# Kernel optimization log

Measured on AMD Instinct MI355X. Metric: run time of the kernel, lower is better.

## Reference

```python
import jax, jax.numpy as jnp
import numpy as np
from jax import lax

H = 128
N = 4096


def gru_cell(x, h, Wih, Whh, bih, bhh):
    # PyTorch GRU gate order: r, z, n
    gi = x @ Wih + bih
    gh = h @ Whh + bhh
    ir, iz, inn = jnp.split(gi, 3, axis=-1)
    hr, hz, hn = jnp.split(gh, 3, axis=-1)
    r = jax.nn.sigmoid(ir + hr)
    z = jax.nn.sigmoid(iz + hz)
    n = jnp.tanh(inn + r * hn)
    return (1.0 - z) * n + z * h


def setup_inputs() -> dict:
    key = jax.random.key(0)
    ks = jax.random.split(key, 32)
    s = 0.02
    rn = lambda k, shp, sc=s: (jax.random.normal(k, shp, jnp.float32) * sc)
    inp = {
        'boxes_feature': jax.random.normal(ks[0], (1, N, 1024), jnp.float32),
        'boxes_box_score': jax.random.normal(ks[1], (1, N, 2560), jnp.float32),
        'boxes_box': jax.random.normal(ks[2], (1, N, 320), jnp.float32),
        'boxes_label': jax.random.uniform(ks[3], (1, N), jnp.float32),
        'boxes_weight': jax.random.uniform(ks[4], (1, N), jnp.float32),
        'boxes_num': N,
        'W_appear': rn(ks[5], (1024, H)), 'b_appear': jnp.zeros((H,), jnp.float32),
        'W_s1': rn(ks[6], (2560, 512)), 'b_s1': jnp.zeros((512,), jnp.float32),
        'W_s2': rn(ks[7], (512, H)), 'b_s2': jnp.zeros((H,), jnp.float32),
        'W_box': rn(ks[8], (320, H)), 'b_box': jnp.zeros((H,), jnp.float32),
        'W_all': rn(ks[9], (3 * H, H)), 'b_all': jnp.zeros((H,), jnp.float32),
        'enc_Wih': rn(ks[10], (H, 3 * H)), 'enc_Whh': rn(ks[11], (H, 3 * H)),
        'enc_bih': jnp.zeros((3 * H,), jnp.float32), 'enc_bhh': jnp.zeros((3 * H,), jnp.float32),
        'dec_Wih': rn(ks[12], (H, 3 * H)), 'dec_Whh': rn(ks[13], (H, 3 * H)),
        'dec_bih': jnp.zeros((3 * H,), jnp.float32), 'dec_bhh': jnp.zeros((3 * H,), jnp.float32),
        'W_attn': rn(ks[14], (2 * H, 1)), 'b_attn': jnp.zeros((1,), jnp.float32),
        'W_comb': rn(ks[15], (2 * H, H)), 'b_comb': jnp.zeros((H,), jnp.float32),
        'W_out': rn(ks[16], (H, 1)), 'b_out': jnp.zeros((1,), jnp.float32),
    }
    return inp


def reference(boxes_feature, boxes_box_score, boxes_box, boxes_label, boxes_weight, boxes_num,
              W_appear, b_appear, W_s1, b_s1, W_s2, b_s2, W_box, b_box, W_all, b_all,
              enc_Wih, enc_Whh, enc_bih, enc_bhh, dec_Wih, dec_Whh, dec_bih, dec_bhh,
              W_attn, b_attn, W_comb, b_comb, W_out, b_out):
    n = boxes_num
    h = W_appear.shape[1]
    # per-proposal feature fusion
    ef = jax.nn.relu(boxes_feature[0, :n] @ W_appear + b_appear)            # [N, h]
    es = jax.nn.relu((boxes_box_score[0, :n] @ W_s1 + b_s1) @ W_s2 + b_s2)  # [N, h]
    eb = jax.nn.relu(boxes_box[0, :n] @ W_box + b_box)                       # [N, h]
    X = jax.nn.relu(jnp.concatenate([ef, es, eb], axis=1) @ W_all + b_all)   # [N, h]

    # encoder GRU over proposals (batch=1)
    def enc_step(hc, x):
        hn = gru_cell(x, hc, enc_Wih, enc_Whh, enc_bih, enc_bhh)
        return hn, hn
    h0 = jnp.zeros((h,), X.dtype)
    h_enc, E = lax.scan(enc_step, h0, X)  # E: [N, h]

    # Bahdanau-style attention; NOTE: original softmaxes each [1,1] score over
    # dim=1, so every weight is exactly 1.0. We keep softmax for faithful grads.
    Xw = X @ W_attn[h:]  # [N, 1], constant part of the attn score

    def dec_step(hc, x):
        scores = hc @ W_attn[:h] + b_attn + Xw          # [N, 1]
        w = jax.nn.softmax(scores, axis=1)              # [N, 1] == all ones
        applied = w[:, 0] @ E                           # [h]
        din = jax.nn.relu(jnp.concatenate([x, applied]) @ W_comb + b_comb)
        hn = gru_cell(din, hc, dec_Wih, dec_Whh, dec_bih, dec_bhh)
        return hn, hn

    _, D = lax.scan(dec_step, h_enc, X)  # D: [N, h]
    output = jax.nn.sigmoid(D @ W_out + b_out)  # [N, 1]
    return output, boxes_label[0, :n], boxes_weight[0, :n]
```

## Files before the change

### kernel.cpp

```cpp
#include <hip/hip_runtime.h>
#include <hip/hip_bf16.h>
#include <math.h>

#define NBOX 4096
#define HDIM 128
#define G3   384
#define PF   8

typedef _Float16 half2v __attribute__((ext_vector_type(2)));
typedef short bf16x8 __attribute__((ext_vector_type(8)));
typedef float f32x4 __attribute__((ext_vector_type(4)));
#define LDK 40

__device__ __forceinline__ float sigm(float x) { return 1.f / (1.f + expf(-x)); }
__device__ __forceinline__ float sigm_fast(float x) {
    return __builtin_amdgcn_rcpf(1.f + __expf(-x));
}
__device__ __forceinline__ float tanh_fast(float x) {
    x = fminf(15.f, fmaxf(-15.f, x));
    const float e2 = __expf(2.f * x);
    return (e2 - 1.f) * __builtin_amdgcn_rcpf(e2 + 1.f);
}
__device__ __forceinline__ float bcast_q1(float x) {
    return __int_as_float(__builtin_amdgcn_mov_dpp(__float_as_int(x), 0x55, 0xF, 0xF, false));
}
__device__ __forceinline__ float bcast_q3(float x) {
    return __int_as_float(__builtin_amdgcn_mov_dpp(__float_as_int(x), 0xFF, 0xF, 0xF, false));
}
__device__ __forceinline__ float qsum(float v) {
    v += __int_as_float(__builtin_amdgcn_mov_dpp(__float_as_int(v), 0xB1, 0xF, 0xF, false));
    v += __int_as_float(__builtin_amdgcn_mov_dpp(__float_as_int(v), 0x4E, 0xF, 0xF, false));
    return v;
}
__device__ __forceinline__ float fdot2(unsigned int h2, unsigned int w2, float acc) {
    return __builtin_amdgcn_fdot2(__builtin_bit_cast(half2v, h2),
                                  __builtin_bit_cast(half2v, w2), acc, false);
}
__device__ __forceinline__ void bar_lds() {
    asm volatile("s_waitcnt lgkmcnt(0)\n\ts_barrier" ::: "memory");
}
__device__ __forceinline__ unsigned short f2bf(float x) {
    return __builtin_bit_cast(unsigned short, __float2bfloat16(x));
}

__global__ __launch_bounds__(256) void gemm_f32(
    const float* __restrict__ A, const float* __restrict__ B,
    const float* __restrict__ bias, float* __restrict__ C,
    int M, int N, int K, int ldc, int act)
{
    __shared__ float As[16][132];
    __shared__ float Bs[16][68];
    const int tid = threadIdx.x;
    const int m0 = blockIdx.y * 128;
    const int n0 = blockIdx.x * 64;
    const int ak = tid & 15, am = tid >> 4;
    const int bn = tid & 63, bk = tid >> 6;
    const int tx = tid & 15, ty = tid >> 4;
    float acc[8][4] = {};
    for (int k0 = 0; k0 < K; k0 += 16) {
#pragma unroll
        for (int r = 0; r < 8; ++r)
            As[ak][am + 16 * r] = A[(size_t)(m0 + am + 16 * r) * K + k0 + ak];
#pragma unroll
        for (int r = 0; r < 4; ++r)
            Bs[bk + 4 * r][bn] = B[(size_t)(k0 + bk + 4 * r) * N + n0 + bn];
        __syncthreads();
#pragma unroll
        for (int k = 0; k < 16; ++k) {
            float4 a0 = *(const float4*)&As[k][ty * 8];
            float4 a1 = *(const float4*)&As[k][ty * 8 + 4];
            float4 b0 = *(const float4*)&Bs[k][tx * 4];
            float a[8] = {a0.x, a0.y, a0.z, a0.w, a1.x, a1.y, a1.z, a1.w};
            float b[4] = {b0.x, b0.y, b0.z, b0.w};
#pragma unroll
            for (int i = 0; i < 8; ++i)
#pragma unroll
                for (int j = 0; j < 4; ++j)
                    acc[i][j] = fmaf(a[i], b[j], acc[i][j]);
        }
        __syncthreads();
    }
#pragma unroll
    for (int i = 0; i < 8; ++i) {
        const int m = m0 + ty * 8 + i;
#pragma unroll
        for (int j = 0; j < 4; ++j) {
            const int n = n0 + tx * 4 + j;
            float v = acc[i][j] + bias[n];
            if (act) v = fmaxf(v, 0.f);
            C[(size_t)m * ldc + n] = v;
        }
    }
}

__global__ __launch_bounds__(256) void conv_bt(
    const float* __restrict__ B, unsigned short* __restrict__ Bt, int K, int N)
{
    const int id = blockIdx.x * 256 + threadIdx.x;
    if (id < K * N) {
        const int n = id / K, k = id % K;
        Bt[(size_t)n * K + k] = f2bf(B[(size_t)k * N + n]);
    }
}

__global__ __launch_bounds__(256) void gemm_bf16t(
    const float* __restrict__ A, const unsigned short* __restrict__ Bt,
    const float* __restrict__ bias, float* __restrict__ C,
    int M, int N, int K, int ldc, int act)
{
    __shared__ unsigned short As[128][LDK];
    __shared__ unsigned short Bs[128][LDK];
    const int tid = threadIdx.x;
    const int m0 = blockIdx.y * 128, n0 = blockIdx.x * 128;
    const int wv = tid >> 6, lane = tid & 63;
    const int wr = (wv >> 1) * 64, wc = (wv & 1) * 64;
    const int lr = lane & 15, lk = lane >> 4;
    const int sm = tid >> 1, skh = (tid & 1) * 16;
    f32x4 acc[4][4] = {};
    for (int k0 = 0; k0 < K; k0 += 32) {
        const float* ga = &A[(size_t)(m0 + sm) * K + k0 + skh];
        float4 f0 = *(const float4*)(ga + 0);
        float4 f1 = *(const float4*)(ga + 4);
        float4 f2 = *(const float4*)(ga + 8);
        float4 f3 = *(const float4*)(ga + 12);
        const float fa[16] = {f0.x,f0.y,f0.z,f0.w, f1.x,f1.y,f1.z,f1.w,
                              f2.x,f2.y,f2.z,f2.w, f3.x,f3.y,f3.z,f3.w};
        unsigned int pk[8];
#pragma unroll
        for (int e = 0; e < 8; ++e)
            pk[e] = (unsigned int)f2bf(fa[2*e]) | ((unsigned int)f2bf(fa[2*e+1]) << 16);
        *(uint4*)&As[sm][skh]     = make_uint4(pk[0], pk[1], pk[2], pk[3]);
        *(uint4*)&As[sm][skh + 8] = make_uint4(pk[4], pk[5], pk[6], pk[7]);
        const uint4* gb = (const uint4*)&Bt[(size_t)(n0 + sm) * K + k0 + skh];
        *(uint4*)&Bs[sm][skh]     = gb[0];
        *(uint4*)&Bs[sm][skh + 8] = gb[1];
        __syncthreads();
        bf16x8 af[4], bfr[4];
#pragma unroll
        for (int f = 0; f < 4; ++f) {
            af[f]  = *(const bf16x8*)&As[wr + f * 16 + lr][lk * 8];
            bfr[f] = *(const bf16x8*)&Bs[wc + f * 16 + lr][lk * 8];
        }
#pragma unroll
        for (int i = 0; i < 4; ++i)
#pragma unroll
            for (int j = 0; j < 4; ++j)
                acc[i][j] = __builtin_amdgcn_mfma_f32_16x16x32_bf16(
                    af[i], bfr[j], acc[i][j], 0, 0, 0);
        __syncthreads();
    }
#pragma unroll
    for (int i = 0; i < 4; ++i)
#pragma unroll
        for (int j = 0; j < 4; ++j)
#pragma unroll
            for (int r = 0; r < 4; ++r) {
                const int row = m0 + wr + i * 16 + lk * 4 + r;
                const int col = n0 + wc + j * 16 + lr;
                float v = acc[i][j][r] + bias[col];
                if (act) v = fmaxf(v, 0.f);
                C[(size_t)row * ldc + col] = v;
            }
}

__global__ __launch_bounds__(256)
__attribute__((amdgpu_waves_per_eu(1, 1)))
void gru_scan(
    const float* __restrict__ GI, const float* __restrict__ Whh,
    const float* __restrict__ bhh, const float* __restrict__ h0,
    double* __restrict__ esum_out, float* __restrict__ hfinal_out,
    float* __restrict__ D_out, int T)
{
    __shared__ unsigned short h16[2][HDIM];
    const int tid = threadIdx.x;
    const int j = tid >> 2;
    const int g = tid & 3;
    const int qa = 2 * j, qb = 2 * j + 1;
    const int myq = (g & 2) ? qb : qa;
    const int colS = ((g & 1) ? HDIM : 0) + myq;
    const int colT = 2 * HDIM + myq;
    unsigned int w[96];
#pragma unroll
    for (int c6 = 0; c6 < 6; ++c6) {
        const int cc = (c6 % 3) * HDIM + ((c6 < 3) ? qa : qb);
#pragma unroll
        for (int p2 = 0; p2 < 16; ++p2) {
            const int k = 32 * g + 2 * p2;
            const _Float16 lo = (_Float16)Whh[(size_t)k * G3 + cc];
            const _Float16 hi = (_Float16)Whh[(size_t)(k + 1) * G3 + cc];
            w[c6 * 16 + p2] = (unsigned int)__builtin_bit_cast(unsigned short, lo)
                            | ((unsigned int)__builtin_bit_cast(unsigned short, hi) << 16);
        }
    }
#pragma unroll
    for (int p = 0; p < 96; ++p) asm volatile("" : "+v"(w[p]));
    const float bS = bhh[colS];
    const float bT = bhh[colT];
    if (tid < HDIM)
        h16[0][tid] = __builtin_bit_cast(unsigned short,
                                         (_Float16)(h0 ? h0[tid] : 0.f));
    float hp = (float)(_Float16)(h0 ? h0[myq] : 0.f);
    double esum = 0.0;
    float gS[PF], gT[PF], gSn[PF], gTn[PF];
#pragma unroll
    for (int p = 0; p < PF; ++p) {
        gS[p] = GI[(size_t)p * G3 + colS];
        gT[p] = GI[(size_t)p * G3 + colT];
    }
    __syncthreads();
    for (int t0 = 0; t0 < T; t0 += PF) {
#pragma unroll
        for (int p = 0; p < PF; ++p) {
            gSn[p] = GI[(size_t)(t0 + PF + p) * G3 + colS];
            gTn[p] = GI[(size_t)(t0 + PF + p) * G3 + colT];
        }
#pragma unroll
        for (int p = 0; p < PF; ++p) {
            const int t = t0 + p;
            const uint4* hb = (const uint4*)h16[t & 1];
            uint4 uu[4];
#pragma unroll
            for (int pp = 0; pp < 4; ++pp) uu[pp] = hb[4 * g + pp];
            float s0 = 0.f, s1 = 0.f, s2 = 0.f, s3 = 0.f, s4 = 0.f, s5 = 0.f;
#pragma unroll
            for (int pp = 0; pp < 4; ++pp) {
                const unsigned int x[4] = {uu[pp].x, uu[pp].y, uu[pp].z, uu[pp].w};
#pragma unroll
                for (int i2 = 0; i2 < 4; ++i2) {
                    const int pi = 4 * pp + i2;
                    s0 = fdot2(x[i2], w[pi], s0);
                    s1 = fdot2(x[i2], w[16 + pi], s1);
                    s2 = fdot2(x[i2], w[32 + pi], s2);
                    s3 = fdot2(x[i2], w[48 + pi], s3);
                    s4 = fdot2(x[i2], w[64 + pi], s4);
                    s5 = fdot2(x[i2], w[80 + pi], s5);
                }
            }
            s0 = qsum(s0); s1 = qsum(s1); s2 = qsum(s2);
            s3 = qsum(s3); s4 = qsum(s4); s5 = qsum(s5);
            const float ghS = ((g & 2) ? ((g & 1) ? s4 : s3)
                                       : ((g & 1) ? s1 : s0)) + bS;
            const float ghT = ((g & 2) ? s5 : s2) + bT;
            const float s = sigm_fast(gS[p] + ghS);
            const float n = tanh_fast(gT[p] + s * ghT);
            const float z1 = bcast_q1(s);
            const float z3 = bcast_q3(s);
            const float z = (g & 2) ? z3 : z1;
            const float hn = z * (hp - n) + n;
            if (!(g & 1)) {
                h16[(t + 1) & 1][myq] =
                    __builtin_bit_cast(unsigned short, (_Float16)hn);
                esum += (double)hn;
                if (D_out) D_out[(size_t)t * HDIM + myq] = hn;
            }
            hp = (float)(_Float16)hn;
            bar_lds();
        }
#pragma unroll
        for (int p = 0; p < PF; ++p) { gS[p] = gSn[p]; gT[p] = gTn[p]; }
    }
    if (!(g & 1)) {
        if (esum_out) esum_out[myq] = esum;
        if (hfinal_out) hfinal_out[myq] = hp;
    }
}

__global__ void prep_dec(const double* __restrict__ esum, const float* __restrict__ W_comb,
                         const float* __restrict__ b_comb, float* __restrict__ c2)
{
    __shared__ double es[HDIM];
    const int j = threadIdx.x;
    es[j] = esum[j];
    __syncthreads();
    double acc = (double)b_comb[j];
    for (int k = 0; k < HDIM; ++k)
        acc += es[k] * (double)W_comb[(HDIM + k) * HDIM + j];
    c2[j] = (float)acc;
}

__global__ __launch_bounds__(256) void out_row(
    const float* __restrict__ D, const float* __restrict__ Wout,
    const float* __restrict__ b_out, float* __restrict__ out)
{
    const int row = (blockIdx.x * 256 + threadIdx.x) >> 6;
    const int lane = threadIdx.x & 63;
    float v = D[(size_t)row * HDIM + lane] * Wout[lane]
            + D[(size_t)row * HDIM + 64 + lane] * Wout[64 + lane];
#pragma unroll
    for (int s = 32; s > 0; s >>= 1) v += __shfl_down(v, s);
    if (lane == 0) out[row] = sigm(v + b_out[0]);
}

__global__ void copy_lw(const float* __restrict__ lab, const float* __restrict__ wt,
                        float* __restrict__ out)
{
    const int i = blockIdx.x * 256 + threadIdx.x;
    if (i < NBOX) { out[NBOX + i] = lab[i]; out[2 * NBOX + i] = wt[i]; }
}

extern "C" void kernel_launch(void* const* d_in, const int* in_sizes, int n_in,
                              void* d_out, int out_size, void* d_ws, size_t ws_size,
                              hipStream_t stream)
{
    const float* boxes_feature = (const float*)d_in[0];
    const float* boxes_score   = (const float*)d_in[1];
    const float* boxes_box     = (const float*)d_in[2];
    const float* boxes_label   = (const float*)d_in[3];
    const float* boxes_weight  = (const float*)d_in[4];
    const float* W_appear = (const float*)d_in[6];
    const float* b_appear = (const float*)d_in[7];
    const float* W_s1     = (const float*)d_in[8];
    const float* b_s1     = (const float*)d_in[9];
    const float* W_s2     = (const float*)d_in[10];
    const float* b_s2     = (const float*)d_in[11];
    const float* W_box    = (const float*)d_in[12];
    const float* b_box    = (const float*)d_in[13];
    const float* W_all    = (const float*)d_in[14];
    const float* b_all    = (const float*)d_in[15];
    const float* enc_Wih  = (const float*)d_in[16];
    const float* enc_Whh  = (const float*)d_in[17];
    const float* enc_bih  = (const float*)d_in[18];
    const float* enc_bhh  = (const float*)d_in[19];
    const float* dec_Wih  = (const float*)d_in[20];
    const float* dec_Whh  = (const float*)d_in[21];
    const float* dec_bih  = (const float*)d_in[22];
    const float* dec_bhh  = (const float*)d_in[23];
    const float* W_comb   = (const float*)d_in[26];
    const float* b_comb   = (const float*)d_in[27];
    const float* W_out    = (const float*)d_in[28];
    const float* b_out    = (const float*)d_in[29];

    float* out = (float*)d_out;
    float* ws = (float*)d_ws;
    size_t o = 0;
    float* T1   = ws + o; o += (size_t)NBOX * 512;
    float* XCAT = ws + o; o += (size_t)NBOX * G3;
    float* X    = ws + o; o += (size_t)NBOX * HDIM;
    float* GIE  = ws + o; o += (size_t)(NBOX + PF) * G3;
    float* GID  = ws + o; o += (size_t)(NBOX + PF) * G3;
    float* DIN  = ws + o; o += (size_t)NBOX * HDIM;
    float* D    = ws + o; o += (size_t)NBOX * HDIM;
    o = (o + 1) & ~(size_t)1;
    double* esum = (double*)(ws + o); o += 256;
    float* henc = ws + o; o += 128;
    float* c2   = ws + o; o += 128;
    unsigned short* Wt_bf = (unsigned short*)GIE;

    conv_bt<<<(2560 * 512 + 255) / 256, 256, 0, stream>>>(W_s1, Wt_bf, 2560, 512);
    gemm_bf16t<<<dim3(512 / 128, NBOX / 128), 256, 0, stream>>>(
        boxes_score, Wt_bf, b_s1, T1, NBOX, 512, 2560, 512, 0);
    gemm_f32<<<dim3(HDIM / 64, NBOX / 128), 256, 0, stream>>>(
        boxes_feature, W_appear, b_appear, XCAT + 0, NBOX, HDIM, 1024, G3, 1);
    gemm_f32<<<dim3(HDIM / 64, NBOX / 128), 256, 0, stream>>>(
        T1, W_s2, b_s2, XCAT + HDIM, NBOX, HDIM, 512, G3, 1);
    gemm_f32<<<dim3(HDIM / 64, NBOX / 128), 256, 0, stream>>>(
        boxes_box, W_box, b_box, XCAT + 2 * HDIM, NBOX, HDIM, 320, G3, 1);
    gemm_f32<<<dim3(HDIM / 64, NBOX / 128), 256, 0, stream>>>(
        XCAT, W_all, b_all, X, NBOX, HDIM, G3, HDIM, 1);

    gemm_f32<<<dim3(G3 / 64, NBOX / 128), 256, 0, stream>>>(
        X, enc_Wih, enc_bih, GIE, NBOX, G3, HDIM, G3, 0);
    gru_scan<<<1, 256, 0, stream>>>(GIE, enc_Whh, enc_bhh, nullptr,
                                    esum, henc, nullptr, NBOX);

    prep_dec<<<1, 128, 0, stream>>>(esum, W_comb, b_comb, c2);
    gemm_f32<<<dim3(HDIM / 64, NBOX / 128), 256, 0, stream>>>(
        X, W_comb, c2, DIN, NBOX, HDIM, HDIM, HDIM, 1);
    gemm_f32<<<dim3(G3 / 64, NBOX / 128), 256, 0, stream>>>(
        DIN, dec_Wih, dec_bih, GID, NBOX, G3, HDIM, G3, 0);

    gru_scan<<<1, 256, 0, stream>>>(GID, dec_Whh, dec_bhh, henc,
                                    nullptr, nullptr, D, NBOX);

    out_row<<<NBOX / 4, 256, 0, stream>>>(D, W_out, b_out, out);
    copy_lw<<<NBOX / 256, 256, 0, stream>>>(boxes_label, boxes_weight, out);
}
```

Measured before the change: 3.851 ms.

## Move all projection GEMMs to bf16 MFMA path and fuse epilogue kernels

Replaces every fp32 SIMT GEMM (appearance, score, box, combine, input-gate projections) with the existing bf16 transposed-weight MFMA GEMM, adding transposition/conversion launches for each weight into reused workspace buffers. It also merges the output-row and label/weight copy kernels into one launch. This targets the feed-forward GEMM time and launch overhead, at the cost of bf16 precision in the projections and extra conversion launches; the sequential GRU scans are unchanged.

```diff
diff --git a/kernel.cpp b/kernel.cpp
--- a/kernel.cpp
+++ b/kernel.cpp
@@ -41,56 +41,6 @@
 }
 __device__ __forceinline__ unsigned short f2bf(float x) {
     return __builtin_bit_cast(unsigned short, __float2bfloat16(x));
-}
-
-__global__ __launch_bounds__(256) void gemm_f32(
-    const float* __restrict__ A, const float* __restrict__ B,
-    const float* __restrict__ bias, float* __restrict__ C,
-    int M, int N, int K, int ldc, int act)
-{
-    __shared__ float As[16][132];
-    __shared__ float Bs[16][68];
-    const int tid = threadIdx.x;
-    const int m0 = blockIdx.y * 128;
-    const int n0 = blockIdx.x * 64;
-    const int ak = tid & 15, am = tid >> 4;
-    const int bn = tid & 63, bk = tid >> 6;
-    const int tx = tid & 15, ty = tid >> 4;
-    float acc[8][4] = {};
-    for (int k0 = 0; k0 < K; k0 += 16) {
-#pragma unroll
-        for (int r = 0; r < 8; ++r)
-            As[ak][am + 16 * r] = A[(size_t)(m0 + am + 16 * r) * K + k0 + ak];
-#pragma unroll
-        for (int r = 0; r < 4; ++r)
-            Bs[bk + 4 * r][bn] = B[(size_t)(k0 + bk + 4 * r) * N + n0 + bn];
-        __syncthreads();
-#pragma unroll
-        for (int k = 0; k < 16; ++k) {
-            float4 a0 = *(const float4*)&As[k][ty * 8];
-            float4 a1 = *(const float4*)&As[k][ty * 8 + 4];
-            float4 b0 = *(const float4*)&Bs[k][tx * 4];
-            float a[8] = {a0.x, a0.y, a0.z, a0.w, a1.x, a1.y, a1.z, a1.w};
-            float b[4] = {b0.x, b0.y, b0.z, b0.w};
-#pragma unroll
-            for (int i = 0; i < 8; ++i)
-#pragma unroll
-                for (int j = 0; j < 4; ++j)
-                    acc[i][j] = fmaf(a[i], b[j], acc[i][j]);
-        }
-        __syncthreads();
-    }
-#pragma unroll
-    for (int i = 0; i < 8; ++i) {
-        const int m = m0 + ty * 8 + i;
-#pragma unroll
-        for (int j = 0; j < 4; ++j) {
-            const int n = n0 + tx * 4 + j;
-            float v = acc[i][j] + bias[n];
-            if (act) v = fmaxf(v, 0.f);
-            C[(size_t)m * ldc + n] = v;
-        }
-    }
 }
 
 __global__ __launch_bounds__(256) void conv_bt(
@@ -278,24 +228,24 @@
     c2[j] = (float)acc;
 }
 
-__global__ __launch_bounds__(256) void out_row(
+__global__ __launch_bounds__(256) void epilogue(
     const float* __restrict__ D, const float* __restrict__ Wout,
-    const float* __restrict__ b_out, float* __restrict__ out)
-{
-    const int row = (blockIdx.x * 256 + threadIdx.x) >> 6;
-    const int lane = threadIdx.x & 63;
-    float v = D[(size_t)row * HDIM + lane] * Wout[lane]
-            + D[(size_t)row * HDIM + 64 + lane] * Wout[64 + lane];
-#pragma unroll
-    for (int s = 32; s > 0; s >>= 1) v += __shfl_down(v, s);
-    if (lane == 0) out[row] = sigm(v + b_out[0]);
-}
-
-__global__ void copy_lw(const float* __restrict__ lab, const float* __restrict__ wt,
-                        float* __restrict__ out)
-{
-    const int i = blockIdx.x * 256 + threadIdx.x;
-    if (i < NBOX) { out[NBOX + i] = lab[i]; out[2 * NBOX + i] = wt[i]; }
+    const float* __restrict__ b_out, const float* __restrict__ lab,
+    const float* __restrict__ wt, float* __restrict__ out)
+{
+    const int bid = blockIdx.x;
+    if (bid < 1024) {
+        const int row = (bid * 256 + threadIdx.x) >> 6;
+        const int lane = threadIdx.x & 63;
+        float v = D[(size_t)row * HDIM + lane] * Wout[lane]
+                + D[(size_t)row * HDIM + 64 + lane] * Wout[64 + lane];
+#pragma unroll
+        for (int s = 32; s > 0; s >>= 1) v += __shfl_down(v, s);
+        if (lane == 0) out[row] = sigm(v + b_out[0]);
+    } else {
+        const int i = (bid - 1024) * 256 + threadIdx.x;
+        out[NBOX + i] = (i < NBOX) ? lab[i] : wt[i - NBOX];
+    }
 }
 
 extern "C" void kernel_launch(void* const* d_in, const int* in_sizes, int n_in,
@@ -344,34 +294,50 @@
     double* esum = (double*)(ws + o); o += 256;
     float* henc = ws + o; o += 128;
     float* c2   = ws + o; o += 128;
-    unsigned short* Wt_bf = (unsigned short*)GIE;
-
-    conv_bt<<<(2560 * 512 + 255) / 256, 256, 0, stream>>>(W_s1, Wt_bf, 2560, 512);
-    gemm_bf16t<<<dim3(512 / 128, NBOX / 128), 256, 0, stream>>>(
-        boxes_score, Wt_bf, b_s1, T1, NBOX, 512, 2560, 512, 0);
-    gemm_f32<<<dim3(HDIM / 64, NBOX / 128), 256, 0, stream>>>(
-        boxes_feature, W_appear, b_appear, XCAT + 0, NBOX, HDIM, 1024, G3, 1);
-    gemm_f32<<<dim3(HDIM / 64, NBOX / 128), 256, 0, stream>>>(
-        T1, W_s2, b_s2, XCAT + HDIM, NBOX, HDIM, 512, G3, 1);
-    gemm_f32<<<dim3(HDIM / 64, NBOX / 128), 256, 0, stream>>>(
-        boxes_box, W_box, b_box, XCAT + 2 * HDIM, NBOX, HDIM, 320, G3, 1);
-    gemm_f32<<<dim3(HDIM / 64, NBOX / 128), 256, 0, stream>>>(
-        XCAT, W_all, b_all, X, NBOX, HDIM, G3, HDIM, 1);
-
-    gemm_f32<<<dim3(G3 / 64, NBOX / 128), 256, 0, stream>>>(
-        X, enc_Wih, enc_bih, GIE, NBOX, G3, HDIM, G3, 0);
+
+    unsigned short* ws1t  = (unsigned short*)GIE;
+    unsigned short* wappt = ws1t + 1310720;
+    unsigned short* ws2t  = wappt + 131072;
+    unsigned short* wboxt = ws2t + 65536;
+    unsigned short* wallt = wboxt + 40960;
+    unsigned short* encwt = (unsigned short*)GID;
+    unsigned short* wcombt = encwt + 49152;
+    unsigned short* decwt = (unsigned short*)D;
+
+    conv_bt<<<(2560*512 + 255)/256, 256, 0, stream>>>(W_s1,    ws1t,  2560, 512);
+    conv_bt<<<(1024*128 + 255)/256, 256, 0, stream>>>(W_appear, wappt, 1024, 128);
+    conv_bt<<<( 512*128 + 255)/256, 256, 0, stream>>>(W_s2,    ws2t,   512, 128);
+    conv_bt<<<( 320*128 + 255)/256, 256, 0, stream>>>(W_box,   wboxt,  320, 128);
+    conv_bt<<<( 384*128 + 255)/256, 256, 0, stream>>>(W_all,   wallt,  384, 128);
+    conv_bt<<<( 128*384 + 255)/256, 256, 0, stream>>>(enc_Wih, encwt,  128, 384);
+    conv_bt<<<( 128*128 + 255)/256, 256, 0, stream>>>(W_comb,  wcombt, 128, 128);
+    conv_bt<<<( 128*384 + 255)/256, 256, 0, stream>>>(dec_Wih, decwt,  128, 384);
+
+    gemm_bf16t<<<dim3(4, 32), 256, 0, stream>>>(
+        boxes_score, ws1t, b_s1, T1, NBOX, 512, 2560, 512, 0);
+    gemm_bf16t<<<dim3(1, 32), 256, 0, stream>>>(
+        boxes_feature, wappt, b_appear, XCAT + 0, NBOX, 128, 1024, G3, 1);
+    gemm_bf16t<<<dim3(1, 32), 256, 0, stream>>>(
+        T1, ws2t, b_s2, XCAT + HDIM, NBOX, 128, 512, G3, 1);
+    gemm_bf16t<<<dim3(1, 32), 256, 0, stream>>>(
+        boxes_box, wboxt, b_box, XCAT + 2 * HDIM, NBOX, 128, 320, G3, 1);
+    gemm_bf16t<<<dim3(1, 32), 256, 0, stream>>>(
+        XCAT, wallt, b_all, X, NBOX, 128, 384, HDIM, 1);
+
+    gemm_bf16t<<<dim3(3, 32), 256, 0, stream>>>(
+        X, encwt, enc_bih, GIE, NBOX, 384, 128, G3, 0);
     gru_scan<<<1, 256, 0, stream>>>(GIE, enc_Whh, enc_bhh, nullptr,
                                     esum, henc, nullptr, NBOX);
 
     prep_dec<<<1, 128, 0, stream>>>(esum, W_comb, b_comb, c2);
-    gemm_f32<<<dim3(HDIM / 64, NBOX / 128), 256, 0, stream>>>(
-        X, W_comb, c2, DIN, NBOX, HDIM, HDIM, HDIM, 1);
-    gemm_f32<<<dim3(G3 / 64, NBOX / 128), 256, 0, stream>>>(
-        DIN, dec_Wih, dec_bih, GID, NBOX, G3, HDIM, G3, 0);
+    gemm_bf16t<<<dim3(1, 32), 256, 0, stream>>>(
+        X, wcombt, c2, DIN, NBOX, 128, 128, HDIM, 1);
+    gemm_bf16t<<<dim3(3, 32), 256, 0, stream>>>(
+        DIN, decwt, dec_bih, GID, NBOX, 384, 128, G3, 0);
 
     gru_scan<<<1, 256, 0, stream>>>(GID, dec_Whh, dec_bhh, henc,
                                     nullptr, nullptr, D, NBOX);
 
-    out_row<<<NBOX / 4, 256, 0, stream>>>(D, W_out, b_out, out);
-    copy_lw<<<NBOX / 256, 256, 0, stream>>>(boxes_label, boxes_weight, out);
-}
+    epilogue<<<1024 + 32, 256, 0, stream>>>(D, W_out, b_out,
+                                            boxes_label, boxes_weight, out);
+}
```

Result: faster. 3.603 ms (-6.4%).
